# Performance work log

Measured on AMD Instinct MI355X. Metric: run time of the kernel, lower is better.

## Reference

```python
import jax, jax.numpy as jnp
import numpy as np

EOS_COEF = 0.25
NEG_FILL = -1000000.0


def move_lineup(pred_legal_mat, pred_quality_vec, target_legal_mat):
    """Vectorized equivalent of the serial torch move_lineup.

    Key insight: the 'word' encoding w = i + 64*j is a bijection on (i, j), so a
    target move word matches a predicted move word iff they occupy the SAME (i, j)
    cell.  torch.nonzero enumerates in row-major order, so the target index t_idx
    is the row-major rank among target ones, and p_idx is the row-major rank among
    predicted positives at the same cell.
    """
    B, Q = pred_quality_vec.shape
    N = 64 * 64
    t = (target_legal_mat == 1).reshape(B, N)           # [B, 4096] bool
    p = (pred_legal_mat > 0).reshape(B, N)              # [B, 4096] bool
    t_rank = jnp.cumsum(t.astype(jnp.int32), axis=1) - 1  # rank among targets
    p_rank = jnp.cumsum(p.astype(jnp.int32), axis=1) - 1  # rank among preds
    # original: match only if found in preds and p_idx < Q-1 (last slot reserved)
    valid = t & p & (p_rank < Q - 1) & (t_rank < Q)
    p_safe = jnp.clip(p_rank, 0, Q - 1)
    vals = jnp.take_along_axis(pred_quality_vec, p_safe, axis=1)  # [B, N]
    t_safe = jnp.where(valid, jnp.clip(t_rank, 0, Q - 1), Q - 1)
    rows = jnp.broadcast_to(jnp.arange(B)[:, None], (B, N))
    # scatter-max: valid ranks are unique per batch; invalid entries carry -inf
    lined = jnp.full((B, Q), NEG_FILL, pred_quality_vec.dtype)
    lined = lined.at[rows, t_safe].max(jnp.where(valid, vals, -jnp.inf))
    lined = lined.at[:, -1].set(pred_quality_vec[:, -1])
    match = jnp.zeros((B, Q), jnp.float32)
    match = match.at[rows, t_safe].max(valid.astype(jnp.float32))
    match = match.at[:, -1].set(1.0)
    return lined, match


def cross_entropy_gen(inp, target):
    # faithful to the torch version: sum over BATCH dim 0, mean over class dim
    lse = jax.scipy.special.logsumexp(inp, axis=1)                      # [B]
    tn = target / (jnp.sum(target, axis=1, keepdims=True) + 1e-10)      # [B, C]
    return jnp.mean(-jnp.sum(tn * (inp - lse[:, None]), axis=0))


def criterion(pred_legal_mat, pred_quality_vec, target_legal_mat, target_quality_vec):
    # ---- label_loss: weighted BCEWithLogits over the flattened legality map ----
    x = pred_legal_mat.reshape(-1)
    tflat = target_legal_mat.reshape(-1)
    w = jnp.where(tflat == 0, EOS_COEF, 1.0)
    bce = jnp.maximum(x, 0.0) - x * tflat + jnp.log1p(jnp.exp(-jnp.abs(x)))
    loss_labels = jnp.mean(w * bce)
    # ---- mse_score_loss ----
    lined, match = move_lineup(pred_legal_mat, pred_quality_vec, target_legal_mat)
    tq = target_quality_vec * match
    loss_ce = cross_entropy_gen(lined[:, :-1], tq[:, :-1])
    loss_mse = jnp.mean((lined[:, -1] - tq[:, -1]) ** 2)
    loss_score = loss_ce * 200.0 + loss_mse
    return jnp.stack([loss_labels, loss_score])


def setup_inputs() -> dict:
    key = jax.random.key(0)
    k1, k2, k3, k4 = jax.random.split(key, 4)
    B, Q = 4096, 256
    pred_legal_mat = jax.random.normal(k1, (B, 64, 64), jnp.float32) - 2.5
    pred_quality_vec = jax.random.normal(k2, (B, Q), jnp.float32)
    # ~33 legal target moves per board (chess-like sparsity), values in {0, 1}
    target_legal_mat = (jax.random.uniform(k3, (B, 64, 64)) < 0.008).astype(jnp.float32)
    target_quality_vec = jax.random.uniform(k4, (B, Q), jnp.float32)
    return {
        "pred_legal_mat": pred_legal_mat,
        "pred_quality_vec": pred_quality_vec,
        "target_legal_mat": target_legal_mat,
        "target_quality_vec": target_quality_vec,
    }


def reference(pred_legal_mat, pred_quality_vec, target_legal_mat, target_quality_vec):
    return criterion(pred_legal_mat, pred_quality_vec, target_legal_mat, target_quality_vec)
```

## Files before the change

kernel.cpp:

```cpp
#include <hip/hip_runtime.h>
#include <cstdint>
#include <cstddef>

#define NEG_FILL -1000000.0f

__global__ __launch_bounds__(256, 4) void criterion_rows(
    const float* __restrict__ pred_legal,
    const float* __restrict__ pred_quality,
    const float* __restrict__ target_legal,
    const float* __restrict__ target_quality,
    float* __restrict__ partials, int B) {

    const int tid  = threadIdx.x;
    const int lane = tid & 63;
    const int w    = tid >> 6;
    const int rloc = w >> 1;
    const int half = w & 1;
    const int row_raw = blockIdx.x * 2 + rloc;
    const bool active = row_raw < B;
    const int row = active ? row_raw : (B - 1);

    __shared__ float lined[2][256];
    __shared__ float matchv[2][256];
    __shared__ int   scnt[4][3];
    __shared__ float sbce[4];
    __shared__ int   sent[4][8];

    {
        float* lp = &lined[0][0];
        float* mp = &matchv[0][0];
        lp[tid] = NEG_FILL; lp[tid + 256] = NEG_FILL;
        mp[tid] = 0.0f;     mp[tid + 256] = 0.0f;
    }

    const float* __restrict__ xrow  = pred_legal     + (size_t)row * 4096 + half * 2048;
    const float* __restrict__ trow  = target_legal   + (size_t)row * 4096 + half * 2048;
    const float* __restrict__ pqrow = pred_quality   + (size_t)row * 256;
    const float* __restrict__ tqrow = target_quality + (size_t)row * 256;

    float4 xb[8], tb[8];
    #pragma unroll
    for (int i = 0; i < 8; ++i) {
        xb[i] = *(const float4*)(xrow + i * 256 + lane * 4);
        tb[i] = *(const float4*)(trow + i * 256 + lane * 4);
    }

    float bce = 0.0f;
    int t_run = 0, p_run = 0, nm = 0;

    #pragma unroll
    for (int seg = 0; seg < 8; ++seg) {
        const float4 x4 = xb[seg];
        const float4 t4 = tb[seg];
        const float xs[4] = {x4.x, x4.y, x4.z, x4.w};
        const float ts[4] = {t4.x, t4.y, t4.z, t4.w};

        uint64_t bt[4], bp[4];
        #pragma unroll
        for (int e = 0; e < 4; ++e) {
            const float x = xs[e], t = ts[e];
            const float a  = __builtin_fabsf(x);
            const float p2 = __builtin_amdgcn_exp2f(a * -1.44269504f);
            const float L  = __builtin_amdgcn_logf(1.0f + p2) * 0.69314718f;
            const float relu = fmaxf(x, 0.0f);
            const float wgt  = 0.25f + 0.75f * t;
            bce += wgt * (relu - x * t + L);
            bt[e] = __ballot(t == 1.0f);
            bp[e] = __ballot(x > 0.0f);
        }

        const uint64_t bm0 = bt[0] & bp[0], bm1 = bt[1] & bp[1];
        const uint64_t bm2 = bt[2] & bp[2], bm3 = bt[3] & bp[3];
        if ((bm0 | bm1 | bm2 | bm3) != 0ull) {
            const uint64_t bms[4] = {bm0, bm1, bm2, bm3};
            #pragma unroll
            for (int e = 0; e < 4; ++e) {
                uint64_t m = bms[e];
                while (m) {
                    const int j = (int)__builtin_ctzll(m);
                    m &= m - 1;
                    const uint64_t below = (j == 0) ? 0ull : ((~0ull) >> (64 - j));
                    int ltr = t_run, lpr = p_run;
                    #pragma unroll
                    for (int e2 = 0; e2 < 4; ++e2) {
                        ltr += (int)__popcll(bt[e2] & below);
                        lpr += (int)__popcll(bp[e2] & below);
                        if (e2 < e) {
                            ltr += (int)((bt[e2] >> j) & 1ull);
                            lpr += (int)((bp[e2] >> j) & 1ull);
                        }
                    }
                    if (ltr < 256 && lpr < 255 && nm < 8) {
                        if (lane == 0) sent[w][nm] = (ltr << 8) | lpr;
                        ++nm;
                    }
                }
            }
        }
        t_run += (int)(__popcll(bt[0]) + __popcll(bt[1])
                     + __popcll(bt[2]) + __popcll(bt[3]));
        p_run += (int)(__popcll(bp[0]) + __popcll(bp[1])
                     + __popcll(bp[2]) + __popcll(bp[3]));
    }

    #pragma unroll
    for (int off = 32; off > 0; off >>= 1)
        bce += __shfl_xor(bce, off, 64);

    if (lane == 0) {
        scnt[w][0] = t_run; scnt[w][1] = p_run; scnt[w][2] = nm;
        sbce[w] = bce;
    }
    __syncthreads();

    {
        const int w0 = rloc * 2;
        int baseT = 0, baseP = 0;
        if (half == 1) { baseT = scnt[w0][0]; baseP = scnt[w0][1]; }
        const int mynm = scnt[w][2];
        for (int i = 0; i < mynm; ++i) {
            const int ent = sent[w][i];
            const int tr = baseT + (ent >> 8);
            const int pr = baseP + (ent & 0xFF);
            if (tr < 256 && pr < 255) {
                if (lane == 0) {
                    lined[rloc][tr]  = pqrow[pr];
                    matchv[rloc][tr] = 1.0f;
                }
            }
        }
    }
    __syncthreads();

    if (half == 0) {
        float vs[4], tq[4];
        #pragma unroll
        for (int k = 0; k < 4; ++k) {
            const int c = k * 64 + lane;
            vs[k] = lined[rloc][c];
            tq[k] = tqrow[c] * matchv[rloc][c];
        }
        if (lane == 63) { vs[3] = -3.0e38f; tq[3] = 0.0f; }

        float m = fmaxf(fmaxf(vs[0], vs[1]), fmaxf(vs[2], vs[3]));
        #pragma unroll
        for (int off = 32; off > 0; off >>= 1)
            m = fmaxf(m, __shfl_xor(m, off, 64));

        float s1 = 0.0f, s2 = 0.0f, s3 = 0.0f;
        #pragma unroll
        for (int k = 0; k < 4; ++k) {
            s1 += __builtin_amdgcn_exp2f((vs[k] - m) * 1.44269504f);
            s2 += tq[k];
            s3 += tq[k] * vs[k];
        }
        #pragma unroll
        for (int off = 32; off > 0; off >>= 1) {
            s1 += __shfl_xor(s1, off, 64);
            s2 += __shfl_xor(s2, off, 64);
            s3 += __shfl_xor(s3, off, 64);
        }

        if (lane == 0 && active) {
            const float s0   = sbce[w] + sbce[w + 1];
            const float lse  = m + __builtin_amdgcn_logf(s1) * 0.69314718f;
            const float csum = -(s3 - lse * s2) / (s2 + 1e-10f);
            const float d    = pqrow[255] - tqrow[255];
            float4 o;
            o.x = s0; o.y = csum; o.z = d * d; o.w = 0.0f;
            *(float4*)(partials + (size_t)row * 4) = o;
        }
    }
}

__global__ __launch_bounds__(256) void finalize_kernel(
    const float* __restrict__ partials, float* __restrict__ out, int B) {
    const int tid = threadIdx.x;
    double s0 = 0.0, s1 = 0.0, s2 = 0.0;
    for (int r = tid; r < B; r += 256) {
        const float4 p = *(const float4*)(partials + (size_t)r * 4);
        s0 += (double)p.x; s1 += (double)p.y; s2 += (double)p.z;
    }
    #pragma unroll
    for (int off = 32; off > 0; off >>= 1) {
        s0 += __shfl_xor(s0, off, 64);
        s1 += __shfl_xor(s1, off, 64);
        s2 += __shfl_xor(s2, off, 64);
    }
    __shared__ double red[3][4];
    const int lane = tid & 63, w = tid >> 6;
    if (lane == 0) { red[0][w] = s0; red[1][w] = s1; red[2][w] = s2; }
    __syncthreads();
    if (tid == 0) {
        const double bs = red[0][0] + red[0][1] + red[0][2] + red[0][3];
        const double cs = red[1][0] + red[1][1] + red[1][2] + red[1][3];
        const double qs = red[2][0] + red[2][1] + red[2][2] + red[2][3];
        out[0] = (float)(bs / ((double)B * 4096.0));
        out[1] = (float)(200.0 * (cs / 255.0) + qs / (double)B);
    }
}

extern "C" void kernel_launch(void* const* d_in, const int* in_sizes, int n_in,
                              void* d_out, int out_size, void* d_ws, size_t ws_size,
                              hipStream_t stream) {
    const float* pred_legal     = (const float*)d_in[0];
    const float* pred_quality   = (const float*)d_in[1];
    const float* target_legal   = (const float*)d_in[2];
    const float* target_quality = (const float*)d_in[3];

    const int B = in_sizes[0] / 4096;

    float* partials = (float*)d_ws;

    const int grid = (B + 1) / 2;
    criterion_rows<<<grid, 256, 0, stream>>>(
        pred_legal, pred_quality, target_legal, target_quality, partials, B);
    finalize_kernel<<<1, 256, 0, stream>>>(partials, (float*)d_out, B);
}
```

Measured before the change: 162.4 us.

## Stage row tiles into LDS via direct global-to-LDS loads, one row per block

```diff
diff --git a/kernel.cpp b/kernel.cpp
--- a/kernel.cpp
+++ b/kernel.cpp
@@ -4,61 +4,62 @@
 
 #define NEG_FILL -1000000.0f
 
-__global__ __launch_bounds__(256, 4) void criterion_rows(
+__device__ __forceinline__ void load16_to_lds(const float* g, float* l) {
+    auto g1 = (const __attribute__((address_space(1))) void*)g;
+    auto l3 = (__attribute__((address_space(3))) void*)(uint32_t)(uintptr_t)l;
+    __builtin_amdgcn_global_load_lds(g1, l3, 16, 0, 0);
+}
+
+__global__ __launch_bounds__(256) void criterion_rows(
     const float* __restrict__ pred_legal,
     const float* __restrict__ pred_quality,
     const float* __restrict__ target_legal,
     const float* __restrict__ target_quality,
     float* __restrict__ partials, int B) {
 
+    const int b    = blockIdx.x;
     const int tid  = threadIdx.x;
     const int lane = tid & 63;
     const int w    = tid >> 6;
-    const int rloc = w >> 1;
-    const int half = w & 1;
-    const int row_raw = blockIdx.x * 2 + rloc;
-    const bool active = row_raw < B;
-    const int row = active ? row_raw : (B - 1);
-
-    __shared__ float lined[2][256];
-    __shared__ float matchv[2][256];
-    __shared__ int   scnt[4][3];
+
+    __shared__ __align__(16) float xs[4096];
+    __shared__ __align__(16) float ts[4096];
+    __shared__ float lined[256];
+    __shared__ float matchv[256];
+    __shared__ int   scnt_t[4], scnt_p[4];
     __shared__ float sbce[4];
     __shared__ int   sent[4][8];
 
-    {
-        float* lp = &lined[0][0];
-        float* mp = &matchv[0][0];
-        lp[tid] = NEG_FILL; lp[tid + 256] = NEG_FILL;
-        mp[tid] = 0.0f;     mp[tid + 256] = 0.0f;
-    }
-
-    const float* __restrict__ xrow  = pred_legal     + (size_t)row * 4096 + half * 2048;
-    const float* __restrict__ trow  = target_legal   + (size_t)row * 4096 + half * 2048;
-    const float* __restrict__ pqrow = pred_quality   + (size_t)row * 256;
-    const float* __restrict__ tqrow = target_quality + (size_t)row * 256;
-
-    float4 xb[8], tb[8];
-    #pragma unroll
-    for (int i = 0; i < 8; ++i) {
-        xb[i] = *(const float4*)(xrow + i * 256 + lane * 4);
-        tb[i] = *(const float4*)(trow + i * 256 + lane * 4);
-    }
+    const float* __restrict__ xrow  = pred_legal     + (size_t)b * 4096;
+    const float* __restrict__ trow  = target_legal   + (size_t)b * 4096;
+    const float* __restrict__ pqrow = pred_quality   + (size_t)b * 256;
+    const float* __restrict__ tqrow = target_quality + (size_t)b * 256;
+
+    #pragma unroll
+    for (int i = 0; i < 4; ++i) {
+        const int off = w * 1024 + i * 256;
+        load16_to_lds(xrow + off + lane * 4, &xs[off]);
+        load16_to_lds(trow + off + lane * 4, &ts[off]);
+    }
+    lined[tid]  = NEG_FILL;
+    matchv[tid] = 0.0f;
+    __syncthreads();
 
     float bce = 0.0f;
     int t_run = 0, p_run = 0, nm = 0;
 
     #pragma unroll
-    for (int seg = 0; seg < 8; ++seg) {
-        const float4 x4 = xb[seg];
-        const float4 t4 = tb[seg];
-        const float xs[4] = {x4.x, x4.y, x4.z, x4.w};
-        const float ts[4] = {t4.x, t4.y, t4.z, t4.w};
+    for (int seg = 0; seg < 4; ++seg) {
+        const int base = w * 1024 + seg * 256 + lane * 4;
+        const float4 x4 = *(const float4*)&xs[base];
+        const float4 t4 = *(const float4*)&ts[base];
+        const float xv[4] = {x4.x, x4.y, x4.z, x4.w};
+        const float tv[4] = {t4.x, t4.y, t4.z, t4.w};
 
         uint64_t bt[4], bp[4];
         #pragma unroll
         for (int e = 0; e < 4; ++e) {
-            const float x = xs[e], t = ts[e];
+            const float x = xv[e], t = tv[e];
             const float a  = __builtin_fabsf(x);
             const float p2 = __builtin_amdgcn_exp2f(a * -1.44269504f);
             const float L  = __builtin_amdgcn_logf(1.0f + p2) * 0.69314718f;
@@ -106,39 +107,35 @@
     #pragma unroll
     for (int off = 32; off > 0; off >>= 1)
         bce += __shfl_xor(bce, off, 64);
-
     if (lane == 0) {
-        scnt[w][0] = t_run; scnt[w][1] = p_run; scnt[w][2] = nm;
-        sbce[w] = bce;
+        scnt_t[w] = t_run; scnt_p[w] = p_run; sbce[w] = bce;
     }
     __syncthreads();
 
     {
-        const int w0 = rloc * 2;
         int baseT = 0, baseP = 0;
-        if (half == 1) { baseT = scnt[w0][0]; baseP = scnt[w0][1]; }
-        const int mynm = scnt[w][2];
-        for (int i = 0; i < mynm; ++i) {
+        #pragma unroll
+        for (int k = 0; k < 4; ++k)
+            if (k < w) { baseT += scnt_t[k]; baseP += scnt_p[k]; }
+        for (int i = 0; i < nm; ++i) {
             const int ent = sent[w][i];
             const int tr = baseT + (ent >> 8);
             const int pr = baseP + (ent & 0xFF);
-            if (tr < 256 && pr < 255) {
-                if (lane == 0) {
-                    lined[rloc][tr]  = pqrow[pr];
-                    matchv[rloc][tr] = 1.0f;
-                }
+            if (tr < 256 && pr < 255 && lane == 0) {
+                lined[tr]  = pqrow[pr];
+                matchv[tr] = 1.0f;
             }
         }
     }
     __syncthreads();
 
-    if (half == 0) {
+    if (w == 0) {
         float vs[4], tq[4];
         #pragma unroll
         for (int k = 0; k < 4; ++k) {
             const int c = k * 64 + lane;
-            vs[k] = lined[rloc][c];
-            tq[k] = tqrow[c] * matchv[rloc][c];
+            vs[k] = lined[c];
+            tq[k] = tqrow[c] * matchv[c];
         }
         if (lane == 63) { vs[3] = -3.0e38f; tq[3] = 0.0f; }
 
@@ -161,14 +158,14 @@
             s3 += __shfl_xor(s3, off, 64);
         }
 
-        if (lane == 0 && active) {
-            const float s0   = sbce[w] + sbce[w + 1];
+        if (lane == 0) {
+            const float s0   = (sbce[0] + sbce[1]) + (sbce[2] + sbce[3]);
             const float lse  = m + __builtin_amdgcn_logf(s1) * 0.69314718f;
             const float csum = -(s3 - lse * s2) / (s2 + 1e-10f);
             const float d    = pqrow[255] - tqrow[255];
             float4 o;
             o.x = s0; o.y = csum; o.z = d * d; o.w = 0.0f;
-            *(float4*)(partials + (size_t)row * 4) = o;
+            *(float4*)(partials + (size_t)b * 4) = o;
         }
     }
 }
@@ -212,8 +209,7 @@
 
     float* partials = (float*)d_ws;
 
-    const int grid = (B + 1) / 2;
-    criterion_rows<<<grid, 256, 0, stream>>>(
+    criterion_rows<<<B, 256, 0, stream>>>(
         pred_legal, pred_quality, target_legal, target_quality, partials, B);
     finalize_kernel<<<1, 256, 0, stream>>>(partials, (float*)d_out, B);
 }
```

Result: faster. 158.1 us (-2.6%).
